# Optimization experiments

Hardware: AMD Instinct MI355X
Metric: run time of the kernel (lower is better)

## Reference

```python
import jax, jax.numpy as jnp
import numpy as np

B, T, H = 8, 2048, 512


def _minimaxn(x):
    # global min-max normalization (NetTransform.minimaxn)
    mx = jnp.max(x)
    mn = jnp.min(x)
    return (x - mn) / (mx - mn)


def _fb(e):
    # NetTransform.fb, mode='batch', vectorized over the batch.
    # e: (B, 1, T) -> (B, 1, T, T)
    # Result: out[b,0,i,j] = prod(e[b,0,j:i]) for i>j, 1 on diag, 0 above diag.
    x = e[:, 0]                                   # (B, T)
    Bsz, Tsz = x.shape
    X = jnp.broadcast_to(x[:, :, None], (Bsz, Tsz, Tsz))  # xs = x.unsqueeze(-1).repeat(1,1,T)
    tril1 = jnp.tril(jnp.ones((Tsz, Tsz), x.dtype))
    m_f = jnp.triu(jnp.ones((Tsz, Tsz), x.dtype), 1)
    A = X * tril1 + m_f                           # tril(x) + m_f
    C = jnp.cumprod(A, axis=1)                    # cumprod along dim -2
    S = jnp.concatenate([jnp.ones((Bsz, 1, Tsz), x.dtype), C[:, :-1]], axis=1) - m_f
    return S[:, None]                             # (B, 1, T, T)


def _clustering(energy_t):
    # NetTransform.clustering (tnum == 1), vectorized over batch.
    # energy_t: (B, 1, T) -> bool mask (B, 1, T) with top-num_neg of (1-energy) set True
    x = 1.0 - energy_t[:, 0]                      # (B, T)
    num_neg = x.sum(-1).astype(jnp.int32)         # int() truncation; x >= 0 so == floor
    ranks = jnp.argsort(jnp.argsort(-x, axis=-1), axis=-1)  # rank 0 = largest
    m = ranks < num_neg[:, None]
    return m[:, None]                             # (B, 1, T)


def setup_inputs() -> dict:
    key = jax.random.key(0)
    k1, k2, k3 = jax.random.split(key, 3)
    e = jax.random.uniform(k1, (B, 1, T), dtype=jnp.float32)
    h = jax.random.normal(k2, (B, 1, T, H), dtype=jnp.float32)
    ilens = jnp.concatenate([
        jnp.array([T], dtype=jnp.int32),
        jax.random.randint(k3, (B - 1,), T // 2, T + 1).astype(jnp.int32),
    ])
    return {"e": e, "h": h, "ilens": ilens}


def reference(e, h, ilens):
    sg = jax.lax.stop_gradient
    # energy_t = minimaxn(flows['e']).detach()
    energy_t = sg(_minimaxn(e))                   # (B, 1, T)
    # clustering mask (computed in forward; unused when cutting_gauge == 0)
    _ = _clustering(energy_t)
    # energy_t_cumprod = fb(energy_t)  (under no_grad)
    K = sg(_fb(energy_t))                         # (B, 1, T, T)
    # h_agg = (K @ h) / K.sum(-1, keepdim), then transpose(-2, -1)
    h_agg = jnp.einsum('bnts,bnsh->bnth', K, h) / K.sum(-1, keepdims=True)
    h_agg = jnp.swapaxes(h_agg, -2, -1)           # (B, 1, H, T)
    # kernel = (h @ h_agg.detach() + h.detach() @ h_agg) / 2 / sqrt(H)
    kernel = (jnp.matmul(h, sg(h_agg)) + jnp.matmul(sg(h), h_agg)) / 2.0 / np.sqrt(H).astype(np.float32)
    return kernel                                 # (B, 1, T, T)
```

## Files before the change

kernel.cpp:

```cpp
#include <hip/hip_runtime.h>
#include <hip/hip_bf16.h>
#include <stdint.h>

#define B_DIM 8
#define T_DIM 2048
#define H_DIM 512
#define NC 32
#define LCH 64
#define BM 128
#define BN 128
#define BK 64

typedef float floatx4 __attribute__((ext_vector_type(4)));
typedef __bf16 bf16x8 __attribute__((ext_vector_type(8)));

__global__ __launch_bounds__(1024) void minmax_kernel(const float* __restrict__ e,
                                                      float* __restrict__ stats,
                                                      int* __restrict__ flags) {
    const float4* e4 = (const float4*)e;
    int tid = threadIdx.x;
    if (tid < B_DIM * NC) flags[tid] = 0;
    float mn = 1e30f, mx = -1e30f;
    #pragma unroll
    for (int i = 0; i < 4; ++i) {
        float4 v = e4[tid + i * 1024];
        mn = fminf(mn, fminf(fminf(v.x, v.y), fminf(v.z, v.w)));
        mx = fmaxf(mx, fmaxf(fmaxf(v.x, v.y), fmaxf(v.z, v.w)));
    }
    for (int off = 32; off > 0; off >>= 1) {
        mn = fminf(mn, __shfl_down(mn, off, 64));
        mx = fmaxf(mx, __shfl_down(mx, off, 64));
    }
    __shared__ float smn[16], smx[16];
    int wid = tid >> 6;
    if ((tid & 63) == 0) { smn[wid] = mn; smx[wid] = mx; }
    __syncthreads();
    if (tid == 0) {
        mn = smn[0]; mx = smx[0];
        #pragma unroll
        for (int w = 1; w < 16; ++w) { mn = fminf(mn, smn[w]); mx = fmaxf(mx, smx[w]); }
        stats[0] = mn;
        stats[1] = 1.0f / (mx - mn);
    }
}

__global__ __launch_bounds__(512) void fused_scan_kernel(
        const float* __restrict__ e, const float* __restrict__ h,
        const float* __restrict__ stats,
        __hip_bfloat16* __restrict__ h_bf,
        float* __restrict__ Lend, float* __restrict__ PPend, float* __restrict__ LDend,
        __hip_bfloat16* __restrict__ hagg_bf,
        int* __restrict__ flags) {
    const int b = blockIdx.x, c = blockIdx.y, hd = threadIdx.x;
    const int t0 = c * LCH;
    const float mn = stats[0], sc = stats[1];
    const float* eb = e + b * T_DIM;
    const float* hp = h + ((size_t)b * T_DIM + t0) * H_DIM + hd;
    __hip_bfloat16* hbp = h_bf + ((size_t)b * T_DIM + t0) * H_DIM + hd;
    __hip_bfloat16* hop = hagg_bf + ((size_t)b * T_DIM + t0) * H_DIM + hd;

    float lv = 0.0f, ldv = 0.0f, pp = 1.0f;
    #pragma unroll 8
    for (int i = 0; i < LCH; ++i) {
        int t = t0 + i;
        float a = (t == 0) ? 0.0f : (eb[t - 1] - mn) * sc;
        float hv = hp[(size_t)i * H_DIM];
        lv = fmaf(a, lv, hv);
        ldv = fmaf(a, ldv, 1.0f);
        pp *= a;
        hbp[(size_t)i * H_DIM] = __float2bfloat16(hv);
    }
    Lend[((size_t)b * NC + c) * H_DIM + hd] = lv;
    if (hd == 0) { PPend[b * NC + c] = pp; LDend[b * NC + c] = ldv; }
    __syncthreads();
    if (hd == 0) {
        __threadfence();
        __hip_atomic_store(&flags[b * NC + c], 1, __ATOMIC_RELEASE, __HIP_MEMORY_SCOPE_AGENT);
    }

    if (hd < c) {
        while (__hip_atomic_load(&flags[b * NC + hd], __ATOMIC_ACQUIRE,
                                 __HIP_MEMORY_SCOPE_AGENT) == 0) {
            __builtin_amdgcn_s_sleep(2);
        }
    }
    __syncthreads();
    float s = 0.0f, sdv = 0.0f;
    for (int cp = 0; cp < c; ++cp) {
        float pe = PPend[b * NC + cp];
        s   = fmaf(pe, s,   Lend[((size_t)b * NC + cp) * H_DIM + hd]);
        sdv = fmaf(pe, sdv, LDend[b * NC + cp]);
    }

    #pragma unroll 8
    for (int i = 0; i < LCH; ++i) {
        int t = t0 + i;
        float a = (t == 0) ? 0.0f : (eb[t - 1] - mn) * sc;
        float hv = __bfloat162float(hbp[(size_t)i * H_DIM]);
        s   = fmaf(a, s, hv);
        sdv = fmaf(a, sdv, 1.0f);
        hop[(size_t)i * H_DIM] = __float2bfloat16(s / sdv);
    }
}

__device__ __forceinline__ void async16(const void* g, void* l) {
    __builtin_amdgcn_global_load_lds(
        (__attribute__((address_space(1))) void*)g,
        (__attribute__((address_space(3))) void*)l,
        16, 0, 0);
}

__global__ __launch_bounds__(256) void gemm_kernel(
        const __hip_bfloat16* __restrict__ Abf,
        const __hip_bfloat16* __restrict__ Bbf,
        float* __restrict__ C) {
    __shared__ __align__(16) __hip_bfloat16 As[BM * BK];
    __shared__ __align__(16) __hip_bfloat16 Bs[BN * BK];
    const int b = blockIdx.z;
    const int tm = blockIdx.x * BM;
    const int sn = blockIdx.y * BN;
    const int tid = threadIdx.x;
    const int lane = tid & 63;
    const int wave = tid >> 6;
    const int wm = (wave >> 1) * 64;
    const int wn = (wave & 1) * 64;
    const int l16 = lane & 15;
    const int quad = lane >> 4;

    const int srow = tid >> 3;
    const int sgran = (tid & 7) ^ (srow & 7);
    const __hip_bfloat16* Ag = Abf + ((size_t)b * T_DIM + tm + srow) * H_DIM + sgran * 8;
    const __hip_bfloat16* Bg = Bbf + ((size_t)b * T_DIM + sn + srow) * H_DIM + sgran * 8;
    char* AsB = (char*)As;
    char* BsB = (char*)Bs;

    floatx4 zero = {0.0f, 0.0f, 0.0f, 0.0f};
    floatx4 acc[4][4];
    #pragma unroll
    for (int i = 0; i < 4; ++i)
        #pragma unroll
        for (int j = 0; j < 4; ++j) acc[i][j] = zero;

    for (int kk = 0; kk < H_DIM; kk += BK) {
        __syncthreads();
        #pragma unroll
        for (int q = 0; q < 4; ++q) {
            async16(Ag + (size_t)q * 32 * H_DIM + kk, AsB + q * 4096 + tid * 16);
            async16(Bg + (size_t)q * 32 * H_DIM + kk, BsB + q * 4096 + tid * 16);
        }
        asm volatile("s_waitcnt vmcnt(0)" ::: "memory");
        __syncthreads();

        bf16x8 af[2][4], bfv[2][4];
        #pragma unroll
        for (int ku = 0; ku < 2; ++ku)
            #pragma unroll
            for (int i = 0; i < 4; ++i) {
                int ra = wm + i * 16 + l16;
                int rb = wn + i * 16 + l16;
                int ga = (ku * 4 + quad) ^ (l16 & 7);
                af[ku][i]  = *reinterpret_cast<const bf16x8*>(AsB + ra * 128 + ga * 16);
                bfv[ku][i] = *reinterpret_cast<const bf16x8*>(BsB + rb * 128 + ga * 16);
            }
        #pragma unroll
        for (int ku = 0; ku < 2; ++ku)
            #pragma unroll
            for (int i = 0; i < 4; ++i)
                #pragma unroll
                for (int j = 0; j < 4; ++j)
                    acc[i][j] = __builtin_amdgcn_mfma_f32_16x16x32_bf16(af[ku][i], bfv[ku][j], acc[i][j], 0, 0, 0);
    }

    const float scale = 0.04419417382415922f;
    float* Cp = C + (size_t)b * T_DIM * T_DIM;
    #pragma unroll
    for (int i = 0; i < 4; ++i) {
        int row0 = tm + wm + i * 16 + quad * 4;
        #pragma unroll
        for (int j = 0; j < 4; ++j) {
            int col = sn + wn + j * 16 + l16;
            #pragma unroll
            for (int r = 0; r < 4; ++r)
                Cp[(size_t)(row0 + r) * T_DIM + col] = acc[i][j][r] * scale;
        }
    }
}

extern "C" void kernel_launch(void* const* d_in, const int* in_sizes, int n_in,
                              void* d_out, int out_size, void* d_ws, size_t ws_size,
                              hipStream_t stream) {
    const float* e = (const float*)d_in[0];
    const float* h = (const float*)d_in[1];
    float* out = (float*)d_out;

    char* ws = (char*)d_ws;
    float* stats            = (float*)ws;
    int* flags              = (int*)(ws + 256);
    __hip_bfloat16* h_bf    = (__hip_bfloat16*)(ws + 4096);
    __hip_bfloat16* hagg_bf = (__hip_bfloat16*)(ws + 4096 + (16u << 20));
    char* p = ws + 4096 + (32u << 20);
    float* Lend  = (float*)p;   p += (size_t)B_DIM * NC * H_DIM * 4;
    float* PPend = (float*)p;   p += B_DIM * NC * 4;
    float* LDend = (float*)p;

    minmax_kernel<<<1, 1024, 0, stream>>>(e, stats, flags);
    fused_scan_kernel<<<dim3(B_DIM, NC), 512, 0, stream>>>(
        e, h, stats, h_bf, Lend, PPend, LDend, hagg_bf, flags);
    gemm_kernel<<<dim3(T_DIM / BM, T_DIM / BN, B_DIM), 256, 0, stream>>>(h_bf, hagg_bf, out);
}
```

Baseline: 251.2 us.

## Replace lookback scan with three-pass chunked scan and vectorized subsegments

Splits the fused scan with spin-wait lookback into a chunk-sum kernel, a serial carry kernel over sub-segments, and a rescan kernel. Each thread now processes four hidden columns over a 16-step sub-segment with vector loads, and the normalized energy coefficients are staged in shared memory. This removes inter-block flag polling and shortens per-thread serial chains. It adds two launches and a serial 128-step carry pass run by only eight blocks.

```diff
diff --git a/kernel.cpp b/kernel.cpp
--- a/kernel.cpp
+++ b/kernel.cpp
@@ -7,19 +7,21 @@
 #define H_DIM 512
 #define NC 32
 #define LCH 64
+#define NSUB 4
+#define LSUB 16
+#define NSEG (NC * NSUB)
 #define BM 128
 #define BN 128
 #define BK 64
 
 typedef float floatx4 __attribute__((ext_vector_type(4)));
+typedef __bf16 bf16x4 __attribute__((ext_vector_type(4)));
 typedef __bf16 bf16x8 __attribute__((ext_vector_type(8)));
 
 __global__ __launch_bounds__(1024) void minmax_kernel(const float* __restrict__ e,
-                                                      float* __restrict__ stats,
-                                                      int* __restrict__ flags) {
+                                                      float* __restrict__ stats) {
     const float4* e4 = (const float4*)e;
     int tid = threadIdx.x;
-    if (tid < B_DIM * NC) flags[tid] = 0;
     float mn = 1e30f, mx = -1e30f;
     #pragma unroll
     for (int i = 0; i < 4; ++i) {
@@ -44,62 +46,101 @@
     }
 }
 
-__global__ __launch_bounds__(512) void fused_scan_kernel(
+__global__ __launch_bounds__(512) void chunk_sum_kernel(
         const float* __restrict__ e, const float* __restrict__ h,
         const float* __restrict__ stats,
         __hip_bfloat16* __restrict__ h_bf,
-        float* __restrict__ Lend, float* __restrict__ PPend, float* __restrict__ LDend,
-        __hip_bfloat16* __restrict__ hagg_bf,
-        int* __restrict__ flags) {
-    const int b = blockIdx.x, c = blockIdx.y, hd = threadIdx.x;
-    const int t0 = c * LCH;
-    const float mn = stats[0], sc = stats[1];
-    const float* eb = e + b * T_DIM;
+        float* __restrict__ Lsub, float* __restrict__ PPsub, float* __restrict__ LDsub) {
+    const int b = blockIdx.x, c = blockIdx.y;
+    const int tid = threadIdx.x;
+    const int hdq = tid & 127, sub = tid >> 7;
+    const int hd = hdq * 4;
+    const int t0 = c * LCH + sub * LSUB;
+
+    __shared__ float se[LCH];
+    if (tid < LCH) {
+        int t = c * LCH + tid;
+        se[tid] = (t == 0) ? 0.0f : (e[b * T_DIM + t - 1] - stats[0]) * stats[1];
+    }
+    __syncthreads();
+
     const float* hp = h + ((size_t)b * T_DIM + t0) * H_DIM + hd;
     __hip_bfloat16* hbp = h_bf + ((size_t)b * T_DIM + t0) * H_DIM + hd;
-    __hip_bfloat16* hop = hagg_bf + ((size_t)b * T_DIM + t0) * H_DIM + hd;
-
-    float lv = 0.0f, ldv = 0.0f, pp = 1.0f;
+
+    floatx4 lv = {0.0f, 0.0f, 0.0f, 0.0f};
+    float ldv = 0.0f, pp = 1.0f;
     #pragma unroll 8
-    for (int i = 0; i < LCH; ++i) {
-        int t = t0 + i;
-        float a = (t == 0) ? 0.0f : (eb[t - 1] - mn) * sc;
-        float hv = hp[(size_t)i * H_DIM];
-        lv = fmaf(a, lv, hv);
+    for (int i = 0; i < LSUB; ++i) {
+        float a = se[sub * LSUB + i];
+        floatx4 hv = *(const floatx4*)(hp + (size_t)i * H_DIM);
+        lv = a * lv + hv;
         ldv = fmaf(a, ldv, 1.0f);
         pp *= a;
-        hbp[(size_t)i * H_DIM] = __float2bfloat16(hv);
-    }
-    Lend[((size_t)b * NC + c) * H_DIM + hd] = lv;
-    if (hd == 0) { PPend[b * NC + c] = pp; LDend[b * NC + c] = ldv; }
+        bf16x4 o;
+        #pragma unroll
+        for (int k = 0; k < 4; ++k) o[k] = (__bf16)hv[k];
+        *(bf16x4*)(hbp + (size_t)i * H_DIM) = o;
+    }
+    int seg = (b * NC + c) * NSUB + sub;
+    *(floatx4*)(Lsub + (size_t)seg * H_DIM + hd) = lv;
+    if (hdq == 0) { PPsub[seg] = pp; LDsub[seg] = ldv; }
+}
+
+__global__ __launch_bounds__(512) void carry_kernel(
+        const float* __restrict__ Lsub, const float* __restrict__ PPsub,
+        const float* __restrict__ LDsub,
+        float* __restrict__ Ssub, float* __restrict__ SDsub) {
+    const int b = blockIdx.x, hd = threadIdx.x;
+    float s = 0.0f, sd = 0.0f;
+    #pragma unroll 4
+    for (int g = 0; g < NSEG; ++g) {
+        int seg = b * NSEG + g;
+        Ssub[(size_t)seg * H_DIM + hd] = s;
+        if (hd == 0) SDsub[seg] = sd;
+        float pe = PPsub[seg];
+        s  = fmaf(pe, s,  Lsub[(size_t)seg * H_DIM + hd]);
+        sd = fmaf(pe, sd, LDsub[seg]);
+    }
+}
+
+__global__ __launch_bounds__(512) void rescan_kernel(
+        const float* __restrict__ e, const __hip_bfloat16* __restrict__ h_bf,
+        const float* __restrict__ stats,
+        const float* __restrict__ Ssub, const float* __restrict__ SDsub,
+        __hip_bfloat16* __restrict__ hagg_bf) {
+    const int b = blockIdx.x, c = blockIdx.y;
+    const int tid = threadIdx.x;
+    const int hdq = tid & 127, sub = tid >> 7;
+    const int hd = hdq * 4;
+    const int t0 = c * LCH + sub * LSUB;
+
+    __shared__ float se[LCH];
+    if (tid < LCH) {
+        int t = c * LCH + tid;
+        se[tid] = (t == 0) ? 0.0f : (e[b * T_DIM + t - 1] - stats[0]) * stats[1];
+    }
     __syncthreads();
-    if (hd == 0) {
-        __threadfence();
-        __hip_atomic_store(&flags[b * NC + c], 1, __ATOMIC_RELEASE, __HIP_MEMORY_SCOPE_AGENT);
-    }
-
-    if (hd < c) {
-        while (__hip_atomic_load(&flags[b * NC + hd], __ATOMIC_ACQUIRE,
-                                 __HIP_MEMORY_SCOPE_AGENT) == 0) {
-            __builtin_amdgcn_s_sleep(2);
-        }
-    }
-    __syncthreads();
-    float s = 0.0f, sdv = 0.0f;
-    for (int cp = 0; cp < c; ++cp) {
-        float pe = PPend[b * NC + cp];
-        s   = fmaf(pe, s,   Lend[((size_t)b * NC + cp) * H_DIM + hd]);
-        sdv = fmaf(pe, sdv, LDend[b * NC + cp]);
-    }
-
+
+    const int seg = (b * NC + c) * NSUB + sub;
+    const __hip_bfloat16* hbp = h_bf + ((size_t)b * T_DIM + t0) * H_DIM + hd;
+    __hip_bfloat16* hop = hagg_bf + ((size_t)b * T_DIM + t0) * H_DIM + hd;
+
+    floatx4 s = *(const floatx4*)(Ssub + (size_t)seg * H_DIM + hd);
+    float sd = SDsub[seg];
     #pragma unroll 8
-    for (int i = 0; i < LCH; ++i) {
-        int t = t0 + i;
-        float a = (t == 0) ? 0.0f : (eb[t - 1] - mn) * sc;
-        float hv = __bfloat162float(hbp[(size_t)i * H_DIM]);
-        s   = fmaf(a, s, hv);
-        sdv = fmaf(a, sdv, 1.0f);
-        hop[(size_t)i * H_DIM] = __float2bfloat16(s / sdv);
+    for (int i = 0; i < LSUB; ++i) {
+        float a = se[sub * LSUB + i];
+        bf16x4 hb = *(const bf16x4*)(hbp + (size_t)i * H_DIM);
+        floatx4 hv;
+        #pragma unroll
+        for (int k = 0; k < 4; ++k) hv[k] = (float)hb[k];
+        s = a * s + hv;
+        sd = fmaf(a, sd, 1.0f);
+        float inv = 1.0f / sd;
+        bf16x4 o;
+        #pragma unroll
+        for (int k = 0; k < 4; ++k) o[k] = (__bf16)(s[k] * inv);
+        *(bf16x4*)(hop + (size_t)i * H_DIM) = o;
     }
 }
 
@@ -195,16 +236,18 @@
 
     char* ws = (char*)d_ws;
     float* stats            = (float*)ws;
-    int* flags              = (int*)(ws + 256);
     __hip_bfloat16* h_bf    = (__hip_bfloat16*)(ws + 4096);
     __hip_bfloat16* hagg_bf = (__hip_bfloat16*)(ws + 4096 + (16u << 20));
     char* p = ws + 4096 + (32u << 20);
-    float* Lend  = (float*)p;   p += (size_t)B_DIM * NC * H_DIM * 4;
-    float* PPend = (float*)p;   p += B_DIM * NC * 4;
-    float* LDend = (float*)p;
-
-    minmax_kernel<<<1, 1024, 0, stream>>>(e, stats, flags);
-    fused_scan_kernel<<<dim3(B_DIM, NC), 512, 0, stream>>>(
-        e, h, stats, h_bf, Lend, PPend, LDend, hagg_bf, flags);
+    float* Lsub  = (float*)p;   p += (size_t)B_DIM * NSEG * H_DIM * 4;
+    float* Ssub  = (float*)p;   p += (size_t)B_DIM * NSEG * H_DIM * 4;
+    float* PPsub = (float*)p;   p += B_DIM * NSEG * 4;
+    float* LDsub = (float*)p;   p += B_DIM * NSEG * 4;
+    float* SDsub = (float*)p;
+
+    minmax_kernel<<<1, 1024, 0, stream>>>(e, stats);
+    chunk_sum_kernel<<<dim3(B_DIM, NC), 512, 0, stream>>>(e, h, stats, h_bf, Lsub, PPsub, LDsub);
+    carry_kernel<<<B_DIM, 512, 0, stream>>>(Lsub, PPsub, LDsub, Ssub, SDsub);
+    rescan_kernel<<<dim3(B_DIM, NC), 512, 0, stream>>>(e, h_bf, stats, Ssub, SDsub, hagg_bf);
     gemm_kernel<<<dim3(T_DIM / BM, T_DIM / BN, B_DIM), 256, 0, stream>>>(h_bf, hagg_bf, out);
 }
```

New measurement: 234.1 us. 6.8% less time.
